# Performance work log

Measured on AMD Instinct MI355X. Metric: run time of the kernel, lower is better.

Reference implementation:

```python
import jax, jax.numpy as jnp
import numpy as np

# TT-factorized linear: 784 = 7*4*7*4 -> 512 = 4*4*8*4, max_rank=20
# canonical TT ranks: [1, 20, 20, 16, 1] (r3 capped by m4*n4 = 16)
B = 16384
R1, R2, R3 = 20, 20, 16


def setup_inputs() -> dict:
    key = jax.random.key(0)
    k = jax.random.split(key, 6)
    x = jax.random.normal(k[0], (B, 784), jnp.float32)
    # TT cores G_k[r_{k-1}, m_k, n_k, r_k] with boundary ranks squeezed
    core1 = jax.random.normal(k[1], (7, 4, R1), jnp.float32) * 0.3   # [m1,n1,r1]
    core2 = jax.random.normal(k[2], (R1, 4, 4, R2), jnp.float32) * 0.1  # [r1,m2,n2,r2]
    core3 = jax.random.normal(k[3], (R2, 7, 8, R3), jnp.float32) * 0.05  # [r2,m3,n3,r3]
    core4 = jax.random.normal(k[4], (R3, 4, 4), jnp.float32) * 0.1   # [r3,m4,n4]
    bias = jax.random.normal(k[5], (512,), jnp.float32) * 0.01
    return {"x": x, "core1": core1, "core2": core2, "core3": core3,
            "core4": core4, "bias": bias}


def reference(x, core1, core2, core3, core4, bias):
    b = x.shape[0]
    # reshape input into TT mode factorization [B, m1, m2, m3, m4]
    x5 = x.reshape(b, 7, 4, 7, 4)
    # chain of small core contractions (the fusion-opportunity op pattern)
    t = jnp.einsum('bijkl,ipr->bjklpr', x5, core1)   # [B,4,7,4, n1,r1]
    t = jnp.einsum('bjklpr,rjqs->bklpqs', t, core2)  # [B,7,4, n1,n2,r2]
    t = jnp.einsum('bklpqs,sket->blpqet', t, core3)  # [B,4, n1,n2,n3,r3]
    y = jnp.einsum('blpqet,tlf->bpqef', t, core4)    # [B, n1,n2,n3,n4]
    y = y.reshape(b, 512) + bias
    # original forward: relu then softmax over features.
    # NOTE: the source calls self.fc2(y) but discards the result, so it is
    # omitted here (no effect on output).
    return jax.nn.softmax(jax.nn.relu(y), axis=1)
```

## Files before the change

kernel.cpp:

```cpp
#include <hip/hip_runtime.h>


typedef __attribute__((ext_vector_type(8))) short short8;
typedef __attribute__((ext_vector_type(4))) float floatx4;

#define T123_OFF 0
#define T12_OFF  1605632
#define WP_OFF   1641472

__device__ __forceinline__ unsigned int pack2_bf16(float a, float b) {
    unsigned int ua = __float_as_uint(a);
    unsigned int ub = __float_as_uint(b);
    return ((ub + 0x8000u) & 0xFFFF0000u) | ((ua + 0x8000u) >> 16);
}

__global__ void prep_t12(const float* __restrict__ c1, const float* __restrict__ c2,
                         float* __restrict__ t12) {
    int idx = blockIdx.x * 256 + threadIdx.x;
    if (idx >= 8960) return;
    int s  = idx % 20;
    int pq = (idx / 20) & 15;
    int ij = idx / 320;
    int i = ij >> 2, j2 = ij & 3;
    int p = pq >> 2, q  = pq & 3;
    float acc = 0.f;
    #pragma unroll
    for (int r = 0; r < 20; ++r)
        acc += c1[i * 80 + p * 20 + r] * c2[r * 320 + j2 * 80 + q * 20 + s];
    t12[idx] = acc;
}

__global__ void prep_t123(const float* __restrict__ t12, const float* __restrict__ c3,
                          float* __restrict__ t123) {
    int idx = blockIdx.x * 256 + threadIdx.x;
    if (idx >= 401408) return;
    int t   = idx & 15;
    int pqe = (idx >> 4) & 127;
    int ijk = idx >> 11;
    int k3 = ijk % 7;
    int ij = ijk / 7;
    int e  = pqe & 7;
    int pq = pqe >> 3;
    float acc = 0.f;
    const float* tp = t12 + (ij * 16 + pq) * 20;
    const float* cp = c3 + k3 * 128 + e * 16 + t;
    #pragma unroll
    for (int s = 0; s < 20; ++s)
        acc += tp[s] * cp[s * 896];
    t123[idx] = acc;
}

__global__ void prep_wp(const float* __restrict__ t123, const float* __restrict__ c4,
                        short* __restrict__ wp) {
    int idx = blockIdx.x * 256 + threadIdx.x;
    if (idx >= 409600) return;
    int j    = idx & 7;
    int lane = (idx >> 3) & 63;
    int tkt  = idx >> 9;
    int tk = tkt % 25;
    int tn = tkt / 25;
    int k = tk * 32 + (lane >> 4) * 8 + j;
    int n = tn * 16 + (lane & 15);
    float v = 0.f;
    if (k < 784) {
        int l  = k & 3;
        int k3 = (k >> 2) % 7;
        int ij = k / 28;
        int f4 = n & 3;
        int e  = (n >> 2) & 7;
        int q  = (n >> 5) & 3;
        int p  = n >> 7;
        int ijk = ij * 7 + k3;
        int pqe = p * 32 + q * 8 + e;
        const float* tp = t123 + (size_t)(ijk * 128 + pqe) * 16;
        const float* cp = c4 + l * 4 + f4;
        float a = 0.f;
        #pragma unroll
        for (int t = 0; t < 16; ++t)
            a += tp[t] * cp[t * 16];
        v = a;
    }
    unsigned int u = __float_as_uint(v);
    wp[idx] = (short)(((u + 0x7FFFu + ((u >> 16) & 1)) >> 16) & 0xFFFF);
}

__global__ __launch_bounds__(256, 2) void tt_gemm(const float* __restrict__ x,
                                                  const short* __restrict__ wp,
                                                  const float* __restrict__ bias,
                                                  float* __restrict__ out) {
    const int tid  = threadIdx.x;
    const int w    = tid >> 6;
    const int lane = tid & 63;
    const int quad = lane >> 4;
    const int lid  = lane & 15;
    const int m_base = blockIdx.x * 32;
    const int tn_base = w * 8;

    floatx4 acc[2][8];
    #pragma unroll
    for (int a = 0; a < 2; ++a)
        #pragma unroll
        for (int b = 0; b < 8; ++b)
            acc[a][b] = floatx4{0.f, 0.f, 0.f, 0.f};

    for (int tk = 0; tk < 25; ++tk) {
        const int k0 = tk * 32;
        const int kk = k0 + quad * 8;

        short8 afrag[2];
        #pragma unroll
        for (int mt = 0; mt < 2; ++mt) {
            const int row = m_base + mt * 16 + lid;
            floatx4 v0 = floatx4{0.f, 0.f, 0.f, 0.f};
            floatx4 v1 = floatx4{0.f, 0.f, 0.f, 0.f};
            if (kk < 784) {
                const floatx4* p = (const floatx4*)(x + (size_t)row * 784 + kk);
                v0 = p[0];
                v1 = p[1];
            }
            union { short8 s; unsigned int u[4]; } af;
            af.u[0] = pack2_bf16(v0.x, v0.y);
            af.u[1] = pack2_bf16(v0.z, v0.w);
            af.u[2] = pack2_bf16(v1.x, v1.y);
            af.u[3] = pack2_bf16(v1.z, v1.w);
            afrag[mt] = af.s;
        }

        short8 bfrag[8];
        #pragma unroll
        for (int nt = 0; nt < 8; ++nt)
            bfrag[nt] = *(const short8*)(wp + (((size_t)(tn_base + nt) * 25 + tk) * 64 + lane) * 8);

        #pragma unroll
        for (int nt = 0; nt < 8; ++nt) {
            acc[0][nt] = __builtin_amdgcn_mfma_f32_16x16x32_bf16(afrag[0], bfrag[nt], acc[0][nt], 0, 0, 0);
            acc[1][nt] = __builtin_amdgcn_mfma_f32_16x16x32_bf16(afrag[1], bfrag[nt], acc[1][nt], 0, 0, 0);
        }
    }

    __shared__ float part[4][32];

    float bias_v[8];
    #pragma unroll
    for (int nt = 0; nt < 8; ++nt)
        bias_v[nt] = bias[w * 128 + nt * 16 + lid];

    float rsum[2][4];
    #pragma unroll
    for (int mt = 0; mt < 2; ++mt) {
        #pragma unroll
        for (int reg = 0; reg < 4; ++reg) {
            float s = 0.f;
            #pragma unroll
            for (int nt = 0; nt < 8; ++nt) {
                float v = acc[mt][nt][reg] + bias_v[nt];
                v = fmaxf(v, 0.f);
                float e = __expf(v);
                acc[mt][nt][reg] = e;
                s += e;
            }
            s += __shfl_xor(s, 1, 64);
            s += __shfl_xor(s, 2, 64);
            s += __shfl_xor(s, 4, 64);
            s += __shfl_xor(s, 8, 64);
            rsum[mt][reg] = s;
        }
    }

    if (lid == 0) {
        #pragma unroll
        for (int mt = 0; mt < 2; ++mt)
            #pragma unroll
            for (int reg = 0; reg < 4; ++reg)
                part[w][mt * 16 + quad * 4 + reg] = rsum[mt][reg];
    }
    __syncthreads();

    #pragma unroll
    for (int mt = 0; mt < 2; ++mt) {
        #pragma unroll
        for (int reg = 0; reg < 4; ++reg) {
            const int rl = mt * 16 + quad * 4 + reg;
            const float tot = part[0][rl] + part[1][rl] + part[2][rl] + part[3][rl];
            const float inv = 1.0f / tot;
            const int row_g = m_base + rl;
            #pragma unroll
            for (int nt = 0; nt < 8; ++nt)
                out[(size_t)row_g * 512 + w * 128 + nt * 16 + lid] = acc[mt][nt][reg] * inv;
        }
    }
}

extern "C" void kernel_launch(void* const* d_in, const int* in_sizes, int n_in,
                              void* d_out, int out_size, void* d_ws, size_t ws_size,
                              hipStream_t stream) {
    const float* x    = (const float*)d_in[0];
    const float* c1   = (const float*)d_in[1];
    const float* c2   = (const float*)d_in[2];
    const float* c3   = (const float*)d_in[3];
    const float* c4   = (const float*)d_in[4];
    const float* bias = (const float*)d_in[5];
    float* out = (float*)d_out;

    char* ws = (char*)d_ws;
    float* t123 = (float*)(ws + T123_OFF);
    float* t12  = (float*)(ws + T12_OFF);
    short* wp   = (short*)(ws + WP_OFF);

    prep_t12 <<<35,   256, 0, stream>>>(c1, c2, t12);
    prep_t123<<<1568, 256, 0, stream>>>(t12, c3, t123);
    prep_wp  <<<1600, 256, 0, stream>>>(t123, c4, wp);
    tt_gemm  <<<512,  256, 0, stream>>>(x, wp, bias, out);
}
```

Before: 149.5 us.

## Fuse t12 prep into t123 kernel and retile GEMM to 16-row blocks with prefetch

Drops the separate t12 prep kernel. Each t123 block now recomputes its 320-element t12 slice into shared memory, removing one launch and a global round-trip. The GEMM now runs 1024 blocks of 512 threads, each covering 16 rows across 8 waves of 64 columns, and uses a register double-buffer that loads the next K-slice's A/B fragments before issuing the current MFMAs. The smaller row tile doubles the block count for better CU coverage and lowers per-wave register pressure, but every B fragment is now reused for only one M tile, so weight traffic from cache per output doubles.

```diff
diff --git a/kernel.cpp b/kernel.cpp
--- a/kernel.cpp
+++ b/kernel.cpp
@@ -5,8 +5,7 @@
 typedef __attribute__((ext_vector_type(4))) float floatx4;
 
 #define T123_OFF 0
-#define T12_OFF  1605632
-#define WP_OFF   1641472
+#define WP_OFF   1605632
 
 __device__ __forceinline__ unsigned int pack2_bf16(float a, float b) {
     unsigned int ua = __float_as_uint(a);
@@ -14,40 +13,39 @@
     return ((ub + 0x8000u) & 0xFFFF0000u) | ((ua + 0x8000u) >> 16);
 }
 
-__global__ void prep_t12(const float* __restrict__ c1, const float* __restrict__ c2,
-                         float* __restrict__ t12) {
-    int idx = blockIdx.x * 256 + threadIdx.x;
-    if (idx >= 8960) return;
-    int s  = idx % 20;
-    int pq = (idx / 20) & 15;
-    int ij = idx / 320;
-    int i = ij >> 2, j2 = ij & 3;
-    int p = pq >> 2, q  = pq & 3;
+__global__ void prep_t123(const float* __restrict__ c1, const float* __restrict__ c2,
+                          const float* __restrict__ c3, float* __restrict__ t123) {
+    __shared__ float t12s[320];
+    const int tid = threadIdx.x;
+    const int ijk = blockIdx.x >> 3;
+    const int k3  = ijk % 7;
+    const int ij  = ijk / 7;
+    const int i   = ij >> 2, j2 = ij & 3;
+
+    for (int e = tid; e < 320; e += 256) {
+        int s  = e % 20;
+        int pq = e / 20;
+        int p = pq >> 2, q = pq & 3;
+        float acc = 0.f;
+        #pragma unroll
+        for (int r = 0; r < 20; ++r)
+            acc += c1[i * 80 + p * 20 + r] * c2[r * 320 + j2 * 80 + q * 20 + s];
+        t12s[e] = acc;
+    }
+    __syncthreads();
+
+    const int li  = (blockIdx.x & 7) * 256 + tid;
+    const int t   = li & 15;
+    const int pqe = li >> 4;
+    const int e3  = pqe & 7;
+    const int pq  = pqe >> 3;
     float acc = 0.f;
-    #pragma unroll
-    for (int r = 0; r < 20; ++r)
-        acc += c1[i * 80 + p * 20 + r] * c2[r * 320 + j2 * 80 + q * 20 + s];
-    t12[idx] = acc;
-}
-
-__global__ void prep_t123(const float* __restrict__ t12, const float* __restrict__ c3,
-                          float* __restrict__ t123) {
-    int idx = blockIdx.x * 256 + threadIdx.x;
-    if (idx >= 401408) return;
-    int t   = idx & 15;
-    int pqe = (idx >> 4) & 127;
-    int ijk = idx >> 11;
-    int k3 = ijk % 7;
-    int ij = ijk / 7;
-    int e  = pqe & 7;
-    int pq = pqe >> 3;
-    float acc = 0.f;
-    const float* tp = t12 + (ij * 16 + pq) * 20;
-    const float* cp = c3 + k3 * 128 + e * 16 + t;
+    const float* tp = t12s + pq * 20;
+    const float* cp = c3 + k3 * 128 + e3 * 16 + t;
     #pragma unroll
     for (int s = 0; s < 20; ++s)
         acc += tp[s] * cp[s * 896];
-    t123[idx] = acc;
+    t123[(size_t)ijk * 2048 + li] = acc;
 }
 
 __global__ void prep_wp(const float* __restrict__ t123, const float* __restrict__ c4,
@@ -84,7 +82,7 @@
     wp[idx] = (short)(((u + 0x7FFFu + ((u >> 16) & 1)) >> 16) & 0xFFFF);
 }
 
-__global__ __launch_bounds__(256, 2) void tt_gemm(const float* __restrict__ x,
+__global__ __launch_bounds__(512, 4) void tt_gemm(const float* __restrict__ x,
                                                   const short* __restrict__ wp,
                                                   const float* __restrict__ bias,
                                                   float* __restrict__ out) {
@@ -93,101 +91,92 @@
     const int lane = tid & 63;
     const int quad = lane >> 4;
     const int lid  = lane & 15;
-    const int m_base = blockIdx.x * 32;
-    const int tn_base = w * 8;
-
-    floatx4 acc[2][8];
-    #pragma unroll
-    for (int a = 0; a < 2; ++a)
-        #pragma unroll
-        for (int b = 0; b < 8; ++b)
-            acc[a][b] = floatx4{0.f, 0.f, 0.f, 0.f};
-
+    const int m_base = blockIdx.x * 16;
+
+    const float* xrow = x + (size_t)(m_base + lid) * 784;
+    const short* wpw  = wp + (size_t)w * 4 * 25 * 512 + (lane << 3);
+
+    floatx4 acc[4];
+    #pragma unroll
+    for (int nt = 0; nt < 4; ++nt) acc[nt] = floatx4{0.f, 0.f, 0.f, 0.f};
+
+    auto loadA = [&](int tk) -> short8 {
+        const int kk = tk * 32 + quad * 8;
+        floatx4 v0 = floatx4{0.f, 0.f, 0.f, 0.f};
+        floatx4 v1 = floatx4{0.f, 0.f, 0.f, 0.f};
+        if (kk < 784) {
+            const floatx4* p = (const floatx4*)(xrow + kk);
+            v0 = p[0];
+            v1 = p[1];
+        }
+        union { short8 s; unsigned int u[4]; } af;
+        af.u[0] = pack2_bf16(v0.x, v0.y);
+        af.u[1] = pack2_bf16(v0.z, v0.w);
+        af.u[2] = pack2_bf16(v1.x, v1.y);
+        af.u[3] = pack2_bf16(v1.z, v1.w);
+        return af.s;
+    };
+    auto loadB = [&](int nt, int tk) -> short8 {
+        return *(const short8*)(wpw + (size_t)(nt * 25 + tk) * 512);
+    };
+
+    short8 aC = loadA(0);
+    short8 bC0 = loadB(0, 0), bC1 = loadB(1, 0), bC2 = loadB(2, 0), bC3 = loadB(3, 0);
+
+    #pragma unroll 1
     for (int tk = 0; tk < 25; ++tk) {
-        const int k0 = tk * 32;
-        const int kk = k0 + quad * 8;
-
-        short8 afrag[2];
-        #pragma unroll
-        for (int mt = 0; mt < 2; ++mt) {
-            const int row = m_base + mt * 16 + lid;
-            floatx4 v0 = floatx4{0.f, 0.f, 0.f, 0.f};
-            floatx4 v1 = floatx4{0.f, 0.f, 0.f, 0.f};
-            if (kk < 784) {
-                const floatx4* p = (const floatx4*)(x + (size_t)row * 784 + kk);
-                v0 = p[0];
-                v1 = p[1];
-            }
-            union { short8 s; unsigned int u[4]; } af;
-            af.u[0] = pack2_bf16(v0.x, v0.y);
-            af.u[1] = pack2_bf16(v0.z, v0.w);
-            af.u[2] = pack2_bf16(v1.x, v1.y);
-            af.u[3] = pack2_bf16(v1.z, v1.w);
-            afrag[mt] = af.s;
+        const int tkn = (tk < 24) ? tk + 1 : 0;
+        short8 aN  = loadA(tkn);
+        short8 bN0 = loadB(0, tkn);
+        short8 bN1 = loadB(1, tkn);
+        short8 bN2 = loadB(2, tkn);
+        short8 bN3 = loadB(3, tkn);
+
+        acc[0] = __builtin_amdgcn_mfma_f32_16x16x32_bf16(aC, bC0, acc[0], 0, 0, 0);
+        acc[1] = __builtin_amdgcn_mfma_f32_16x16x32_bf16(aC, bC1, acc[1], 0, 0, 0);
+        acc[2] = __builtin_amdgcn_mfma_f32_16x16x32_bf16(aC, bC2, acc[2], 0, 0, 0);
+        acc[3] = __builtin_amdgcn_mfma_f32_16x16x32_bf16(aC, bC3, acc[3], 0, 0, 0);
+
+        aC = aN; bC0 = bN0; bC1 = bN1; bC2 = bN2; bC3 = bN3;
+    }
+
+    __shared__ float part[8][16];
+
+    float bias_v[4];
+    #pragma unroll
+    for (int nt = 0; nt < 4; ++nt)
+        bias_v[nt] = bias[w * 64 + nt * 16 + lid];
+
+    #pragma unroll
+    for (int reg = 0; reg < 4; ++reg) {
+        float s = 0.f;
+        #pragma unroll
+        for (int nt = 0; nt < 4; ++nt) {
+            float v = acc[nt][reg] + bias_v[nt];
+            v = fmaxf(v, 0.f);
+            float e = __expf(v);
+            acc[nt][reg] = e;
+            s += e;
         }
-
-        short8 bfrag[8];
-        #pragma unroll
-        for (int nt = 0; nt < 8; ++nt)
-            bfrag[nt] = *(const short8*)(wp + (((size_t)(tn_base + nt) * 25 + tk) * 64 + lane) * 8);
-
-        #pragma unroll
-        for (int nt = 0; nt < 8; ++nt) {
-            acc[0][nt] = __builtin_amdgcn_mfma_f32_16x16x32_bf16(afrag[0], bfrag[nt], acc[0][nt], 0, 0, 0);
-            acc[1][nt] = __builtin_amdgcn_mfma_f32_16x16x32_bf16(afrag[1], bfrag[nt], acc[1][nt], 0, 0, 0);
-        }
-    }
-
-    __shared__ float part[4][32];
-
-    float bias_v[8];
-    #pragma unroll
-    for (int nt = 0; nt < 8; ++nt)
-        bias_v[nt] = bias[w * 128 + nt * 16 + lid];
-
-    float rsum[2][4];
-    #pragma unroll
-    for (int mt = 0; mt < 2; ++mt) {
-        #pragma unroll
-        for (int reg = 0; reg < 4; ++reg) {
-            float s = 0.f;
-            #pragma unroll
-            for (int nt = 0; nt < 8; ++nt) {
-                float v = acc[mt][nt][reg] + bias_v[nt];
-                v = fmaxf(v, 0.f);
-                float e = __expf(v);
-                acc[mt][nt][reg] = e;
-                s += e;
-            }
-            s += __shfl_xor(s, 1, 64);
-            s += __shfl_xor(s, 2, 64);
-            s += __shfl_xor(s, 4, 64);
-            s += __shfl_xor(s, 8, 64);
-            rsum[mt][reg] = s;
-        }
-    }
-
-    if (lid == 0) {
-        #pragma unroll
-        for (int mt = 0; mt < 2; ++mt)
-            #pragma unroll
-            for (int reg = 0; reg < 4; ++reg)
-                part[w][mt * 16 + quad * 4 + reg] = rsum[mt][reg];
+        s += __shfl_xor(s, 1, 64);
+        s += __shfl_xor(s, 2, 64);
+        s += __shfl_xor(s, 4, 64);
+        s += __shfl_xor(s, 8, 64);
+        if (lid == 0) part[w][quad * 4 + reg] = s;
     }
     __syncthreads();
 
     #pragma unroll
-    for (int mt = 0; mt < 2; ++mt) {
-        #pragma unroll
-        for (int reg = 0; reg < 4; ++reg) {
-            const int rl = mt * 16 + quad * 4 + reg;
-            const float tot = part[0][rl] + part[1][rl] + part[2][rl] + part[3][rl];
-            const float inv = 1.0f / tot;
-            const int row_g = m_base + rl;
-            #pragma unroll
-            for (int nt = 0; nt < 8; ++nt)
-                out[(size_t)row_g * 512 + w * 128 + nt * 16 + lid] = acc[mt][nt][reg] * inv;
-        }
+    for (int reg = 0; reg < 4; ++reg) {
+        const int rl = quad * 4 + reg;
+        float tot = 0.f;
+        #pragma unroll
+        for (int ww = 0; ww < 8; ++ww) tot += part[ww][rl];
+        const float inv = 1.0f / tot;
+        const size_t row_g = m_base + rl;
+        #pragma unroll
+        for (int nt = 0; nt < 4; ++nt)
+            out[row_g * 512 + w * 64 + nt * 16 + lid] = acc[nt][reg] * inv;
     }
 }
 
@@ -204,11 +193,9 @@
 
     char* ws = (char*)d_ws;
     float* t123 = (float*)(ws + T123_OFF);
-    float* t12  = (float*)(ws + T12_OFF);
     short* wp   = (short*)(ws + WP_OFF);
 
-    prep_t12 <<<35,   256, 0, stream>>>(c1, c2, t12);
-    prep_t123<<<1568, 256, 0, stream>>>(t12, c3, t123);
+    prep_t123<<<1568, 256, 0, stream>>>(c1, c2, c3, t123);
     prep_wp  <<<1600, 256, 0, stream>>>(t123, c4, wp);
-    tt_gemm  <<<512,  256, 0, stream>>>(x, wp, bias, out);
-}
+    tt_gemm  <<<1024, 512, 0, stream>>>(x, wp, bias, out);
+}
```

Measured after the change: 168.7 us. 12.9% more time.
